# Kernel tuning notes

Measured on AMD Instinct MI355X. Metric: run time of the kernel, lower is better.

The kernel has to match this reference:

```python
import jax, jax.numpy as jnp
import numpy as np

# P pipes (padded to common grid), batch B, channels C, grid H x W
P, B, C, H, W = 8, 4, 32, 256, 256
M1, M2 = 32, 32  # retained Fourier modes
SCALE = 1.0 / (C * C)


def setup_inputs() -> dict:
    key = jax.random.key(0)
    ks = jax.random.split(key, 5)
    x = jax.random.normal(ks[0], (P, B, C, H, W), dtype=jnp.float32)
    wshape = (C, C, P, M1, M2)  # (in_ch, out_ch, num_pipe, modes1, modes2)
    w1_re = SCALE * jax.random.uniform(ks[1], wshape, dtype=jnp.float32)
    w1_im = SCALE * jax.random.uniform(ks[2], wshape, dtype=jnp.float32)
    w4_re = SCALE * jax.random.uniform(ks[3], wshape, dtype=jnp.float32)
    w4_im = SCALE * jax.random.uniform(ks[4], wshape, dtype=jnp.float32)
    return {"x": x, "w1_re": w1_re, "w1_im": w1_im, "w4_re": w4_re, "w4_im": w4_im}


def reference(x, w1_re, w1_im, w4_re, w4_im):
    # method == 25 branch of Graph_SpectralConv2d.forward.
    # x: [P, B, C, H, W] (stacked equal-size padded pipes)
    w1 = jax.lax.complex(w1_re, w1_im)  # [C_in, C_out, P, M1, M2], complex64
    w4 = jax.lax.complex(w4_re, w4_im)
    # preprocess: per-pipe 2D rFFT, truncate low / high frequency blocks
    x_ft = jnp.fft.rfftn(x, axes=(3, 4))          # [P, B, C, H, W//2+1]
    fno_in = x_ft[:, :, :, :M1, :M2]              # low-freq block  [P, B, C, M1, M2]
    fno_in_h = x_ft[:, :, :, -M1:, :M2]           # high-freq block [P, B, C, M1, M2]
    # per-pipe complex channel mixing (torch einsum 'bizxy,iozxy->bozxy')
    f_out = jnp.einsum('pbixy,iopxy->pboxy', fno_in, w1)
    f_out_h = jnp.einsum('pbixy,iopxy->pboxy', fno_in_h, w4)
    # postprocess: scatter modes into zero spectrum, inverse rFFT
    wf = W // 2 + 1
    out_ft = jnp.zeros((P, B, C, H, wf), dtype=jnp.complex64)
    out_ft = out_ft.at[:, :, :, :M1, :M2].set(f_out)
    out_ft = out_ft.at[:, :, :, -M1:, :M2].set(f_out_h)
    return jnp.fft.irfftn(out_ft, s=(H, W), axes=(3, 4))  # [P, B, C, H, W] real
```

## Files before the change

kernel.cpp:

```cpp
#include <hip/hip_runtime.h>


constexpr float TWO_PI = 6.28318530717958647692f;

__global__ __launch_bounds__(256) void fwd_dft(const float* __restrict__ x,
                                               float2* __restrict__ X2) {
  __shared__ float2 tw[256];
  __shared__ float u[16][260];
  __shared__ float2 X1[256][16];
  const int t = threadIdx.x;
  {
    float a = (float)t * (TWO_PI / 256.f);
    tw[t] = make_float2(cosf(a), sinf(a));
  }
  const float* xp = x + (size_t)blockIdx.x * 65536;
  const int lane = t & 63, wv = t >> 6;
  const int kxh = lane & 15;
  const int g = lane >> 4;
  const int par = kxh & 1;

  for (int half = 0; half < 2; ++half) {
    const int kx = half * 16 + kxh;
    float2 A[16], Bt[8];
#pragma unroll
    for (int w00 = 0; w00 < 16; ++w00) {
      float a = (TWO_PI / 256.f) * (float)(w00 * kx);
      A[w00] = make_float2(cosf(a), -sinf(a));
    }
#pragma unroll
    for (int w1 = 0; w1 < 8; ++w1) {
      float a = (TWO_PI / 16.f) * (float)(w1 * kxh);
      Bt[w1] = make_float2(cosf(a), -sinf(a));
    }
    for (int chunk = 0; chunk < 16; ++chunk) {
      __syncthreads();
#pragma unroll
      for (int r = 0; r < 2; ++r) {
        int task = t + 256 * r;
        int row = task >> 5;
        int w4 = task & 31;
        const float4 a4 = *(const float4*)(xp + (chunk * 16 + row) * 256 + w4 * 4);
        const float4 b4 = *(const float4*)(xp + (chunk * 16 + row) * 256 + w4 * 4 + 128);
        *(float4*)&u[row][w4 * 8] =
            make_float4(a4.x + b4.x, a4.x - b4.x, a4.y + b4.y, a4.y - b4.y);
        *(float4*)&u[row][w4 * 8 + 4] =
            make_float4(a4.z + b4.z, a4.z - b4.z, a4.w + b4.w, a4.w - b4.w);
      }
      __syncthreads();
      const int hrow = wv * 4 + g;
      const float* up = &u[hrow][par];
      float accx = 0.f, accy = 0.f;
#pragma unroll
      for (int w00 = 0; w00 < 16; ++w00) {
        float Sx = 0.f, Sy = 0.f;
#pragma unroll
        for (int w1 = 0; w1 < 8; ++w1) {
          float uv = up[(w1 * 16 + w00) * 2];
          Sx = fmaf(uv, Bt[w1].x, Sx);
          Sy = fmaf(uv, Bt[w1].y, Sy);
        }
        accx += A[w00].x * Sx - A[w00].y * Sy;
        accy += A[w00].x * Sy + A[w00].y * Sx;
      }
      X1[chunk * 16 + hrow][kxh] = make_float2(accx, accy);
    }
    __syncthreads();
#pragma unroll
    for (int r = 0; r < 8; ++r) {
      int idx = t + 256 * r;
      int h0 = idx >> 4, k = idx & 15;
      float2 a = X1[h0][k], b = X1[h0 + 128][k];
      X1[h0][k] = make_float2(a.x + b.x, a.y + b.y);
      X1[h0 + 128][k] = make_float2(a.x - b.x, a.y - b.y);
    }
    __syncthreads();
    float2* X2p = X2 + (size_t)blockIdx.x * 2048;
    for (int iter = 0; iter < 4; ++iter) {
      int s = wv * 16 + iter * 4 + g;
      int ky = (s < 32) ? s : s + 192;
      const float2* Xrow = &X1[(s & 1) * 128][0];
      float ax = 0.f, ay = 0.f;
#pragma unroll 8
      for (int h0 = 0; h0 < 128; ++h0) {
        float2 v = Xrow[h0 * 16 + kxh];
        float2 z = tw[(h0 * ky) & 255];
        ax += v.x * z.x + v.y * z.y;
        ay += v.y * z.x - v.x * z.y;
      }
      X2p[s * 32 + kx] = make_float2(ax, ay);
    }
    __syncthreads();
  }
}

__global__ __launch_bounds__(256) void mix(const float2* __restrict__ X2,
                                           const float* __restrict__ w1re,
                                           const float* __restrict__ w1im,
                                           const float* __restrict__ w4re,
                                           const float* __restrict__ w4im,
                                           float2* __restrict__ Y2) {
  const int n = blockIdx.x * 256 + threadIdx.x;
  const int kx = n & 31;
  const int s = (n >> 5) & 63;
  const int o = (n >> 11) & 31;
  const int p = n >> 16;
  const float* wre;
  const float* wim;
  int y;
  if (s < 32) { wre = w1re; wim = w1im; y = s; }
  else        { wre = w4re; wim = w4im; y = s - 32; }
  const size_t wbase = (size_t)o * 8192 + (size_t)p * 1024 + y * 32 + kx;
  const size_t in_base = ((size_t)p * 4 * 32) * 2048 + s * 32 + kx;
  float2 acc[4] = {make_float2(0.f, 0.f), make_float2(0.f, 0.f),
                   make_float2(0.f, 0.f), make_float2(0.f, 0.f)};
#pragma unroll 4
  for (int i = 0; i < 32; ++i) {
    const float wr = wre[wbase + (size_t)i * 262144];
    const float wi = wim[wbase + (size_t)i * 262144];
#pragma unroll
    for (int b = 0; b < 4; ++b) {
      float2 v = X2[in_base + (size_t)b * 65536 + (size_t)i * 2048];
      acc[b].x += v.x * wr - v.y * wi;
      acc[b].y += v.x * wi + v.y * wr;
    }
  }
  const size_t out_base = ((size_t)p * 4 * 32 + o) * 2048 + s * 32 + kx;
#pragma unroll
  for (int b = 0; b < 4; ++b) Y2[out_base + (size_t)b * 65536] = acc[b];
}

__global__ __launch_bounds__(256) void inv_dft(const float2* __restrict__ Y2,
                                               float* __restrict__ out) {
  __shared__ float2 tw[256];
  __shared__ float2 Ys[64 * 32];
  __shared__ float2 Y1c[4 * 32 * 32];
  const int t = threadIdx.x;
  {
    float a = (float)t * (TWO_PI / 256.f);
    tw[t] = make_float2(cosf(a), sinf(a));
  }
  {
    const float4* src = (const float4*)(Y2 + (size_t)blockIdx.x * 2048);
    float4* dst = (float4*)Ys;
#pragma unroll
    for (int q = 0; q < 4; ++q) dst[t + 256 * q] = src[t + 256 * q];
  }
  const int lane = t & 63, wv = t >> 6;
  const int kx = lane & 31, hg = lane >> 5;
  const float scale = (kx == 0) ? (1.f / 65536.f) : (2.f / 65536.f);
  float2 T[32];
#pragma unroll
  for (int k = 0; k < 32; ++k) {
    float a = (TWO_PI / 256.f) * (float)(lane * k);
    T[k] = make_float2(cosf(a), sinf(a));
  }
  __syncthreads();
  float* op = out + (size_t)blockIdx.x * 65536;

  for (int pass = 0; pass < 2; ++pass) {
    const int h0base = pass * 32;
    for (int iter = 0; iter < 4; ++iter) {
      const int h0 = h0base + wv * 8 + iter * 2 + hg;
      float B0x = 0, B0y = 0, B1x = 0, B1y = 0;
      float B2x = 0, B2y = 0, B3x = 0, B3y = 0;
#define DSTEP(S, KY, BX, BY)                              \
  {                                                       \
    float2 v = Ys[(S) * 32 + kx];                         \
    float2 z = tw[(h0 * (KY)) & 255];                     \
    BX += v.x * z.x - v.y * z.y;                          \
    BY += v.x * z.y + v.y * z.x;                          \
  }
#pragma unroll 4
      for (int sb = 0; sb < 32; sb += 4) {
        DSTEP(sb + 0, sb + 0, B0x, B0y);
        DSTEP(sb + 1, sb + 1, B1x, B1y);
        DSTEP(sb + 2, sb + 2, B2x, B2y);
        DSTEP(sb + 3, sb + 3, B3x, B3y);
      }
#pragma unroll 4
      for (int sb = 32; sb < 64; sb += 4) {
        DSTEP(sb + 0, sb + 192, B0x, B0y);
        DSTEP(sb + 1, sb + 193, B1x, B1y);
        DSTEP(sb + 2, sb + 194, B2x, B2y);
        DSTEP(sb + 3, sb + 195, B3x, B3y);
      }
#undef DSTEP
      const float Ex = B0x + B2x, Ey = B0y + B2y, Fx = B1x + B3x, Fy = B1y + B3y;
      const float Gx = B0x - B2x, Gy = B0y - B2y, Hx = B1x - B3x, Hy = B1y - B3y;
      float2* yb = &Y1c[(h0 - h0base) * 32 + kx];
      yb[0]    = make_float2((Ex + Fx) * scale, (Ey + Fy) * scale);
      yb[1024] = make_float2((Gx - Hy) * scale, (Gy + Hx) * scale);
      yb[2048] = make_float2((Ex - Fx) * scale, (Ey - Fy) * scale);
      yb[3072] = make_float2((Gx + Hy) * scale, (Gy - Hx) * scale);
    }
    __syncthreads();
    for (int j = 0; j < 32; ++j) {
      const float2* row = &Y1c[wv * 1024 + j * 32];
      float p0 = 0, p2 = 0, P1x = 0, P1y = 0, P3x = 0, P3y = 0;
#pragma unroll
      for (int kb = 0; kb < 32; kb += 4) {
        float4 v01 = *(const float4*)(row + kb);
        float4 v23 = *(const float4*)(row + kb + 2);
        p0  += v01.x * T[kb].x     - v01.y * T[kb].y;
        P1x += v01.z * T[kb + 1].x - v01.w * T[kb + 1].y;
        P1y += v01.z * T[kb + 1].y + v01.w * T[kb + 1].x;
        p2  += v23.x * T[kb + 2].x - v23.y * T[kb + 2].y;
        P3x += v23.z * T[kb + 3].x - v23.w * T[kb + 3].y;
        P3y += v23.z * T[kb + 3].y + v23.w * T[kb + 3].x;
      }
      const int h = wv * 64 + h0base + j;
      float* o = op + h * 256 + lane;
      o[0]   = p0 + P1x + p2 + P3x;
      o[64]  = p0 - P1y - p2 + P3y;
      o[128] = p0 - P1x + p2 - P3x;
      o[192] = p0 + P1y - p2 - P3y;
    }
    __syncthreads();
  }
}

extern "C" void kernel_launch(void* const* d_in, const int* in_sizes, int n_in,
                              void* d_out, int out_size, void* d_ws, size_t ws_size,
                              hipStream_t stream) {
  const float* x = (const float*)d_in[0];
  const float* w1re = (const float*)d_in[1];
  const float* w1im = (const float*)d_in[2];
  const float* w4re = (const float*)d_in[3];
  const float* w4im = (const float*)d_in[4];
  float* out = (float*)d_out;
  float2* X2 = (float2*)d_ws;
  float2* Y2 = X2 + (size_t)1024 * 2048;

  fwd_dft<<<1024, 256, 0, stream>>>(x, X2);
  mix<<<2048, 256, 0, stream>>>(X2, w1re, w1im, w4re, w4im, Y2);
  inv_dft<<<1024, 256, 0, stream>>>(Y2, out);
}
```

Measured before the change: 930.3 us.

## Restructure forward DFT into single pass with register-prefetched chunks and streaming column DFT

Rewrites fwd_dft to drop the two-half loop and the full 256x16 X1 shared buffer. Each block now handles all 32 kx modes in one pass. Global loads for the next chunk are prefetched into registers while the current chunk is computed, and the column DFT is accumulated in registers chunk by chunk instead of running as a separate phase. The A twiddles move to a shared table, and launch bounds request 4 blocks per SM to raise occupancy, at the cost of more register pressure from the 8 accumulators and the prefetch registers.

```diff
diff --git a/kernel.cpp b/kernel.cpp
--- a/kernel.cpp
+++ b/kernel.cpp
@@ -3,94 +3,123 @@
 
 constexpr float TWO_PI = 6.28318530717958647692f;
 
-__global__ __launch_bounds__(256) void fwd_dft(const float* __restrict__ x,
-                                               float2* __restrict__ X2) {
+__global__ __launch_bounds__(256, 4) void fwd_dft(const float* __restrict__ x,
+                                                  float2* __restrict__ X2) {
   __shared__ float2 tw[256];
-  __shared__ float u[16][260];
-  __shared__ float2 X1[256][16];
+  __shared__ float2 At[512];
+  __shared__ __align__(16) float u[2 * 16 * 132];
+  __shared__ float2 buf[16 * 33];
+
   const int t = threadIdx.x;
   {
     float a = (float)t * (TWO_PI / 256.f);
     tw[t] = make_float2(cosf(a), sinf(a));
   }
-  const float* xp = x + (size_t)blockIdx.x * 65536;
-  const int lane = t & 63, wv = t >> 6;
-  const int kxh = lane & 15;
-  const int g = lane >> 4;
-  const int par = kxh & 1;
-
-  for (int half = 0; half < 2; ++half) {
-    const int kx = half * 16 + kxh;
-    float2 A[16], Bt[8];
+#pragma unroll
+  for (int i = 0; i < 2; ++i) {
+    int idx = t + 256 * i;
+    int w00 = idx >> 5, kx = idx & 31;
+    float a = (TWO_PI / 256.f) * (float)(w00 * kx);
+    At[idx] = make_float2(cosf(a), -sinf(a));
+  }
+
+  const int rowA = t >> 4, kxh = t & 15, par = kxh & 1;
+  float2 Bt[8];
+#pragma unroll
+  for (int w1 = 0; w1 < 8; ++w1) {
+    float a = (TWO_PI / 16.f) * (float)(w1 * kxh);
+    Bt[w1] = make_float2(cosf(a), -sinf(a));
+  }
+  const int lrow = t >> 5, w4 = t & 31;
+  const float4* x4 = (const float4*)(x + (size_t)blockIdx.x * 65536);
+  const int sg = t >> 5, kxb = t & 31;
+  const float sgn = (sg & 1) ? -1.f : 1.f;
+  float2 acc[8];
+#pragma unroll
+  for (int j = 0; j < 8; ++j) acc[j] = make_float2(0.f, 0.f);
+
+  float* const U0 = u;
+  float* const U1 = u + 2112;
+  const int ibase = lrow * 132 + 32 * (w4 & 3) + (w4 >> 2);
+  const float* const up = u + par * 2112 + rowA * 132;
+
+  float4 pa0, pb0, pa1, pb1;
+
+#define LOADC(c)                        \
+  {                                     \
+    int h = (c) * 8 + lrow;             \
+    pa0 = x4[h * 64 + w4];              \
+    pb0 = x4[h * 64 + w4 + 32];         \
+    pa1 = x4[(h + 128) * 64 + w4];      \
+    pb1 = x4[(h + 128) * 64 + w4 + 32]; \
+  }
+#define STOREU()                                                      \
+  {                                                                   \
+    U0[ibase] = pa0.x + pb0.x;      U1[ibase] = pa0.x - pb0.x;        \
+    U0[ibase + 8] = pa0.y + pb0.y;  U1[ibase + 8] = pa0.y - pb0.y;    \
+    U0[ibase + 16] = pa0.z + pb0.z; U1[ibase + 16] = pa0.z - pb0.z;   \
+    U0[ibase + 24] = pa0.w + pb0.w; U1[ibase + 24] = pa0.w - pb0.w;   \
+    const int i1 = ibase + 1056;                                      \
+    U0[i1] = pa1.x + pb1.x;      U1[i1] = pa1.x - pb1.x;              \
+    U0[i1 + 8] = pa1.y + pb1.y;  U1[i1 + 8] = pa1.y - pb1.y;          \
+    U0[i1 + 16] = pa1.z + pb1.z; U1[i1 + 16] = pa1.z - pb1.z;         \
+    U0[i1 + 24] = pa1.w + pb1.w; U1[i1 + 24] = pa1.w - pb1.w;         \
+  }
+
+  LOADC(0);
+  STOREU();
+  __syncthreads();
+
+  for (int c = 0; c < 16; ++c) {
+    if (c < 15) LOADC(c + 1);
+    float ax1 = 0.f, ay1 = 0.f, ax2 = 0.f, ay2 = 0.f;
 #pragma unroll
     for (int w00 = 0; w00 < 16; ++w00) {
-      float a = (TWO_PI / 256.f) * (float)(w00 * kx);
-      A[w00] = make_float2(cosf(a), -sinf(a));
-    }
-#pragma unroll
-    for (int w1 = 0; w1 < 8; ++w1) {
-      float a = (TWO_PI / 16.f) * (float)(w1 * kxh);
-      Bt[w1] = make_float2(cosf(a), -sinf(a));
-    }
-    for (int chunk = 0; chunk < 16; ++chunk) {
-      __syncthreads();
-#pragma unroll
-      for (int r = 0; r < 2; ++r) {
-        int task = t + 256 * r;
-        int row = task >> 5;
-        int w4 = task & 31;
-        const float4 a4 = *(const float4*)(xp + (chunk * 16 + row) * 256 + w4 * 4);
-        const float4 b4 = *(const float4*)(xp + (chunk * 16 + row) * 256 + w4 * 4 + 128);
-        *(float4*)&u[row][w4 * 8] =
-            make_float4(a4.x + b4.x, a4.x - b4.x, a4.y + b4.y, a4.y - b4.y);
-        *(float4*)&u[row][w4 * 8 + 4] =
-            make_float4(a4.z + b4.z, a4.z - b4.z, a4.w + b4.w, a4.w - b4.w);
-      }
-      __syncthreads();
-      const int hrow = wv * 4 + g;
-      const float* up = &u[hrow][par];
-      float accx = 0.f, accy = 0.f;
-#pragma unroll
-      for (int w00 = 0; w00 < 16; ++w00) {
-        float Sx = 0.f, Sy = 0.f;
-#pragma unroll
-        for (int w1 = 0; w1 < 8; ++w1) {
-          float uv = up[(w1 * 16 + w00) * 2];
-          Sx = fmaf(uv, Bt[w1].x, Sx);
-          Sy = fmaf(uv, Bt[w1].y, Sy);
-        }
-        accx += A[w00].x * Sx - A[w00].y * Sy;
-        accy += A[w00].x * Sy + A[w00].y * Sx;
-      }
-      X1[chunk * 16 + hrow][kxh] = make_float2(accx, accy);
-    }
+      float4 q0 = *(const float4*)(up + w00 * 8);
+      float4 q1 = *(const float4*)(up + w00 * 8 + 4);
+      float Sx = q0.x + q0.y * Bt[1].x + q0.z * Bt[2].x + q0.w * Bt[3].x +
+                 q1.x * Bt[4].x + q1.y * Bt[5].x + q1.z * Bt[6].x +
+                 q1.w * Bt[7].x;
+      float Sy = q0.y * Bt[1].y + q0.z * Bt[2].y + q0.w * Bt[3].y +
+                 q1.x * Bt[4].y + q1.y * Bt[5].y + q1.z * Bt[6].y +
+                 q1.w * Bt[7].y;
+      float2 A1 = At[w00 * 32 + kxh];
+      float2 A2 = At[w00 * 32 + kxh + 16];
+      ax1 += A1.x * Sx - A1.y * Sy;
+      ay1 += A1.x * Sy + A1.y * Sx;
+      ax2 += A2.x * Sx - A2.y * Sy;
+      ay2 += A2.x * Sy + A2.y * Sx;
+    }
+    buf[rowA * 33 + kxh] = make_float2(ax1, ay1);
+    buf[rowA * 33 + kxh + 16] = make_float2(ax2, ay2);
     __syncthreads();
 #pragma unroll
     for (int r = 0; r < 8; ++r) {
-      int idx = t + 256 * r;
-      int h0 = idx >> 4, k = idx & 15;
-      float2 a = X1[h0][k], b = X1[h0 + 128][k];
-      X1[h0][k] = make_float2(a.x + b.x, a.y + b.y);
-      X1[h0 + 128][k] = make_float2(a.x - b.x, a.y - b.y);
-    }
-    __syncthreads();
-    float2* X2p = X2 + (size_t)blockIdx.x * 2048;
-    for (int iter = 0; iter < 4; ++iter) {
-      int s = wv * 16 + iter * 4 + g;
-      int ky = (s < 32) ? s : s + 192;
-      const float2* Xrow = &X1[(s & 1) * 128][0];
-      float ax = 0.f, ay = 0.f;
-#pragma unroll 8
-      for (int h0 = 0; h0 < 128; ++h0) {
-        float2 v = Xrow[h0 * 16 + kxh];
-        float2 z = tw[(h0 * ky) & 255];
-        ax += v.x * z.x + v.y * z.y;
-        ay += v.y * z.x - v.x * z.y;
-      }
-      X2p[s * 32 + kx] = make_float2(ax, ay);
-    }
-    __syncthreads();
-  }
+      const int h0 = c * 8 + r;
+      float2 a = buf[r * 33 + kxb];
+      float2 b = buf[(r + 8) * 33 + kxb];
+      float vx = fmaf(sgn, b.x, a.x);
+      float vy = fmaf(sgn, b.y, a.y);
+      int tix = h0 * sg;
+      const int h8 = h0 << 3;
+#pragma unroll
+      for (int j = 0; j < 8; ++j) {
+        float2 z = tw[tix & 255];
+        acc[j].x += vx * z.x + vy * z.y;
+        acc[j].y += vy * z.x - vx * z.y;
+        tix += h8;
+        if (j == 3) tix += (h0 << 7) + (h0 << 6);
+      }
+    }
+    if (c < 15) STOREU();
+    __syncthreads();
+  }
+#undef LOADC
+#undef STOREU
+
+  float2* X2p = X2 + (size_t)blockIdx.x * 2048;
+#pragma unroll
+  for (int j = 0; j < 8; ++j) X2p[(sg + 8 * j) * 32 + kxb] = acc[j];
 }
 
 __global__ __launch_bounds__(256) void mix(const float2* __restrict__ X2,
```

Result: slower. 1.357 ms (+45.9%).
